# Performance work log

Measured on AMD Instinct MI355X. Metric: run time of the kernel, lower is better.

## Reference

```python
import jax, jax.numpy as jnp
import numpy as np

D_IN, D_OUT, SEQ = 256, 64, 8192

def setup_inputs() -> dict:
    key = jax.random.key(0)
    kx, kq, kk, kv = jax.random.split(key, 4)
    x = jax.random.normal(kx, (SEQ, D_IN), dtype=jnp.float32)
    # original uses torch.rand (uniform [0,1)) for parameters
    W_q = jax.random.uniform(kq, (D_IN, D_OUT), dtype=jnp.float32)
    W_k = jax.random.uniform(kk, (D_IN, D_OUT), dtype=jnp.float32)
    W_v = jax.random.uniform(kv, (D_IN, D_OUT), dtype=jnp.float32)
    return {"x": x, "W_q": W_q, "W_k": W_k, "W_v": W_v}

def reference(x, W_q, W_k, W_v):
    q = x @ W_q          # [S, d_out]
    k = x @ W_k          # [S, d_out]
    v = x @ W_v          # [S, d_out]
    scores = q @ k.T     # [S, S]
    scale = jnp.asarray(D_OUT, scores.dtype) ** 0.5
    weights = jax.nn.softmax(scores / scale, axis=-1)
    return weights @ v   # [S, d_out]
```

## Files before the change

### kernel.cpp

```cpp
#include <hip/hip_runtime.h>
#include <hip/hip_bf16.h>

#define SEQ   8192
#define DIN   256
#define DOUT  64
#define QSCALE 0.1803368801111204f

using bf16x8 = __attribute__((ext_vector_type(8))) short;
using f32x16 = __attribute__((ext_vector_type(16))) float;

__device__ __forceinline__ float exp2f_fast(float x) { return __builtin_amdgcn_exp2f(x); }

__device__ __forceinline__ f32x16 mfma32(bf16x8 a, bf16x8 b, f32x16 c) {
  return __builtin_amdgcn_mfma_f32_32x32x16_bf16(a, b, c, 0, 0, 0);
}

__device__ __forceinline__ unsigned f2bfbits(float f) {
  unsigned u = __builtin_bit_cast(unsigned, f);
  return (u + 0x7fffu + ((u >> 16) & 1u)) >> 16;
}
__device__ __forceinline__ unsigned pkb(float a, float b) {
  return f2bfbits(a) | (f2bfbits(b) << 16);
}
__device__ __forceinline__ float bfhi_f(float v) {
  return __builtin_bit_cast(float, f2bfbits(v) << 16);
}

__global__ __launch_bounds__(256) void qkv_kernel(
    const float* __restrict__ x, const float* __restrict__ wq,
    const float* __restrict__ wk, const float* __restrict__ wv,
    unsigned short* __restrict__ qhi, unsigned short* __restrict__ qlo,
    unsigned short* __restrict__ khi, unsigned short* __restrict__ klo,
    float* __restrict__ vo)
{
  __shared__ float  sxT[DIN * 32];
  __shared__ float4 sw4[DIN * 8];
  const int tid = threadIdx.x;
  const int r0  = blockIdx.x * 32;

  const float4* x4 = (const float4*)x;
  #pragma unroll
  for (int i = 0; i < 8; ++i) {
    int f4  = tid + 256 * i;
    int row = f4 & 31;
    int d4  = f4 >> 5;
    float4 xv = x4[(size_t)(r0 + row) * 64 + d4];
    sxT[(d4 * 4 + 0) * 32 + row] = xv.x;
    sxT[(d4 * 4 + 1) * 32 + row] = xv.y;
    sxT[(d4 * 4 + 2) * 32 + row] = xv.z;
    sxT[(d4 * 4 + 3) * 32 + row] = xv.w;
  }

  const float* wmats[3] = {wq, wk, wv};
  const int r  = tid >> 3;
  const int cg = tid & 7;

  for (int ph = 0; ph < 6; ++ph) {
    int mat = ph >> 1, ch = ph & 1;
    const float4* w4 = (const float4*)wmats[mat];
    #pragma unroll
    for (int i = 0; i < 8; ++i) {
      int f4 = tid + 256 * i;
      int d  = f4 >> 3, c8 = f4 & 7;
      sw4[d * 8 + c8] = w4[d * 16 + ch * 8 + c8];
    }
    __syncthreads();
    float acc[4] = {0.f, 0.f, 0.f, 0.f};
    for (int d = 0; d < DIN; ++d) {
      float  xv = sxT[d * 32 + r];
      float4 w  = sw4[d * 8 + cg];
      acc[0] = fmaf(xv, w.x, acc[0]); acc[1] = fmaf(xv, w.y, acc[1]);
      acc[2] = fmaf(xv, w.z, acc[2]); acc[3] = fmaf(xv, w.w, acc[3]);
    }
    size_t base = (size_t)(r0 + r) * DOUT + ch * 32 + cg * 4;
    if (mat < 2) {
      if (mat == 0) { acc[0]*=QSCALE; acc[1]*=QSCALE; acc[2]*=QSCALE; acc[3]*=QSCALE; }
      ushort4 hv, lv;
      unsigned short* hp = (unsigned short*)&hv;
      unsigned short* lp = (unsigned short*)&lv;
      #pragma unroll
      for (int j = 0; j < 4; ++j) {
        unsigned hb = f2bfbits(acc[j]);
        hp[j] = (unsigned short)hb;
        float fh = __builtin_bit_cast(float, hb << 16);
        lp[j] = (unsigned short)f2bfbits(acc[j] - fh);
      }
      unsigned short* hdst = mat ? khi : qhi;
      unsigned short* ldst = mat ? klo : qlo;
      *(ushort4*)&hdst[base] = hv;
      *(ushort4*)&ldst[base] = lv;
    } else {
      float4 res = {acc[0], acc[1], acc[2], acc[3]};
      *(float4*)&vo[base] = res;
    }
    __syncthreads();
  }
}

__global__ __launch_bounds__(256) void vtrans_kernel(
    const float* __restrict__ v,
    unsigned short* __restrict__ vThi, unsigned short* __restrict__ vTlo)
{
  __shared__ float t[64][65];
  const int tid = threadIdx.x;
  const int r0  = blockIdx.x * 64;
  #pragma unroll
  for (int i = 0; i < 4; ++i) {
    int flat = tid + 256 * i;
    int row = flat >> 4;
    int c4  = flat & 15;
    float4 w = *(const float4*)&v[(size_t)(r0 + row) * 64 + c4 * 4];
    t[row][c4 * 4 + 0] = w.x; t[row][c4 * 4 + 1] = w.y;
    t[row][c4 * 4 + 2] = w.z; t[row][c4 * 4 + 3] = w.w;
  }
  __syncthreads();
  #pragma unroll
  for (int i = 0; i < 2; ++i) {
    int flat = tid + 256 * i;
    int d   = flat >> 3;
    int seg = flat & 7;
    ushort4 h0, h1, l0, l1;
    unsigned short* hp0 = (unsigned short*)&h0; unsigned short* hp1 = (unsigned short*)&h1;
    unsigned short* lp0 = (unsigned short*)&l0; unsigned short* lp1 = (unsigned short*)&l1;
    #pragma unroll
    for (int j = 0; j < 8; ++j) {
      float val = t[seg * 8 + j][d];
      unsigned hb = f2bfbits(val);
      float fh = __builtin_bit_cast(float, hb << 16);
      unsigned lb = f2bfbits(val - fh);
      if (j < 4) { hp0[j] = (unsigned short)hb; lp0[j] = (unsigned short)lb; }
      else       { hp1[j-4] = (unsigned short)hb; lp1[j-4] = (unsigned short)lb; }
    }
    size_t base = (size_t)d * SEQ + r0 + seg * 8;
    *(ushort4*)&vThi[base]     = h0;
    *(ushort4*)&vThi[base + 4] = h1;
    *(ushort4*)&vTlo[base]     = l0;
    *(ushort4*)&vTlo[base + 4] = l1;
  }
}

__global__ __launch_bounds__(512, 2) void attn_mfma_kernel(
    const unsigned short* __restrict__ qhi, const unsigned short* __restrict__ qlo,
    const unsigned short* __restrict__ khi, const unsigned short* __restrict__ klo,
    const unsigned short* __restrict__ vThi, const unsigned short* __restrict__ vTlo,
    float* __restrict__ opart, float2* __restrict__ mlpart, int slice_len)
{
  __shared__ unsigned short sm[2][4][4096];
  const int tid  = threadIdx.x;
  const int lane = tid & 63;
  const int w    = tid >> 6;
  const int qr   = lane & 31;
  const int h    = lane >> 5;
  const int split = blockIdx.y;
  const int j0   = split * slice_len;
  const int qg   = blockIdx.x * 256 + w * 32 + qr;
  const int NT   = slice_len >> 6;

  bf16x8 qh[4], ql[4];
  #pragma unroll
  for (int c = 0; c < 4; ++c) {
    qh[c] = *(const bf16x8*)&qhi[(size_t)qg * 64 + 16 * c + 8 * h];
    ql[c] = *(const bf16x8*)&qlo[(size_t)qg * 64 + 16 * c + 8 * h];
  }

  f32x16 o0, o1;
  #pragma unroll
  for (int i = 0; i < 16; ++i) { o0[i] = 0.f; o1[i] = 0.f; }
  float m = -1.0e30f, l = 0.f;

  const int srow = tid >> 3, sseg = tid & 7;
  const int soff = srow * 64 + ((sseg ^ (srow & 7)) << 3);

  bf16x8 st[4];
  {
    size_t kr  = (size_t)(j0 + srow);
    size_t col = (size_t)(j0 + sseg * 8);
    st[0] = *(const bf16x8*)&khi[kr * 64 + sseg * 8];
    st[1] = *(const bf16x8*)&klo[kr * 64 + sseg * 8];
    st[2] = *(const bf16x8*)&vThi[(size_t)srow * SEQ + col];
    st[3] = *(const bf16x8*)&vTlo[(size_t)srow * SEQ + col];
    #pragma unroll
    for (int a = 0; a < 4; ++a) *(bf16x8*)&sm[0][a][soff] = st[a];
  }
  __syncthreads();

  for (int t = 0; t < NT; ++t) {
    const int b = t & 1;
    bf16x8 nx[4];
    if (t + 1 < NT) {
      size_t kr  = (size_t)(j0 + (t + 1) * 64 + srow);
      size_t col = (size_t)(j0 + (t + 1) * 64 + sseg * 8);
      nx[0] = *(const bf16x8*)&khi[kr * 64 + sseg * 8];
      nx[1] = *(const bf16x8*)&klo[kr * 64 + sseg * 8];
      nx[2] = *(const bf16x8*)&vThi[(size_t)srow * SEQ + col];
      nx[3] = *(const bf16x8*)&vTlo[(size_t)srow * SEQ + col];
    }
    const unsigned short* KH = &sm[b][0][0];
    const unsigned short* KL = &sm[b][1][0];
    const unsigned short* VH = &sm[b][2][0];
    const unsigned short* VL = &sm[b][3][0];

    f32x16 s0, s1;
    #pragma unroll
    for (int i = 0; i < 16; ++i) { s0[i] = 0.f; s1[i] = 0.f; }
    #pragma unroll
    for (int c = 0; c < 4; ++c) {
      int slot = (2 * c + h) ^ (qr & 7);
      int a0 = qr * 64 + slot * 8;
      int a1 = a0 + 32 * 64;
      bf16x8 kh0 = *(const bf16x8*)&KH[a0];
      bf16x8 kh1 = *(const bf16x8*)&KH[a1];
      bf16x8 kl0 = *(const bf16x8*)&KL[a0];
      bf16x8 kl1 = *(const bf16x8*)&KL[a1];
      s0 = mfma32(kh0, qh[c], s0);
      s1 = mfma32(kh1, qh[c], s1);
      s0 = mfma32(kl0, qh[c], s0);
      s1 = mfma32(kl1, qh[c], s1);
      s0 = mfma32(kh0, ql[c], s0);
      s1 = mfma32(kh1, ql[c], s1);
    }

    float pm = s0[0];
    #pragma unroll
    for (int i = 1; i < 16; ++i) pm = fmaxf(pm, s0[i]);
    #pragma unroll
    for (int i = 0; i < 16; ++i) pm = fmaxf(pm, s1[i]);
    pm = fmaxf(pm, __shfl_xor(pm, 32));

    bool need = (pm > m + 40.0f);
    if (__any(need)) {
      float nm = fmaxf(m, pm);
      float r  = exp2f_fast(m - nm);
      #pragma unroll
      for (int i = 0; i < 16; ++i) { o0[i] *= r; o1[i] *= r; }
      l *= r; m = nm;
    }
    #pragma unroll
    for (int i = 0; i < 16; ++i) { s0[i] = exp2f_fast(s0[i] - m); }
    #pragma unroll
    for (int i = 0; i < 16; ++i) { s1[i] = exp2f_fast(s1[i] - m); }
    float ls = 0.f;
    #pragma unroll
    for (int i = 0; i < 16; ++i) ls += s0[i];
    #pragma unroll
    for (int i = 0; i < 16; ++i) ls += s1[i];
    l += ls + __shfl_xor(ls, 32);

    unsigned fw[4][4];
    #pragma unroll
    for (int ti = 0; ti < 2; ++ti) {
      #pragma unroll
      for (int c = 0; c < 2; ++c) {
        const f32x16& S = ti ? s1 : s0;
        unsigned X0 = pkb(S[8*c+0], S[8*c+1]);
        unsigned Y0 = pkb(S[8*c+2], S[8*c+3]);
        unsigned X1 = pkb(S[8*c+4], S[8*c+5]);
        unsigned Y1 = pkb(S[8*c+6], S[8*c+7]);
        unsigned rX0 = __shfl_xor(X0, 32);
        unsigned rY0 = __shfl_xor(Y0, 32);
        unsigned rX1 = __shfl_xor(X1, 32);
        unsigned rY1 = __shfl_xor(Y1, 32);
        fw[ti*2+c][0] = h ? rX1 : X0;
        fw[ti*2+c][1] = h ? rY1 : Y0;
        fw[ti*2+c][2] = h ? X1  : rX0;
        fw[ti*2+c][3] = h ? Y1  : rY0;
      }
    }

    #pragma unroll
    for (int dt = 0; dt < 2; ++dt) {
      f32x16& O = dt ? o1 : o0;
      #pragma unroll
      for (int kc = 0; kc < 4; ++kc) {
        int slot = (2 * kc + h) ^ (qr & 7);
        int addr = (qr + 32 * dt) * 64 + slot * 8;
        uint4 u = {fw[kc][0], fw[kc][1], fw[kc][2], fw[kc][3]};
        bf16x8 pf = __builtin_bit_cast(bf16x8, u);
        bf16x8 vh = *(const bf16x8*)&VH[addr];
        bf16x8 vl = *(const bf16x8*)&VL[addr];
        O = mfma32(vh, pf, O);
        O = mfma32(vl, pf, O);
      }
    }

    __syncthreads();
    if (t + 1 < NT) {
      #pragma unroll
      for (int a = 0; a < 4; ++a) *(bf16x8*)&sm[b ^ 1][a][soff] = nx[a];
    }
    __syncthreads();
  }

  const size_t obase = ((size_t)split * SEQ + qg) * 64;
  #pragma unroll
  for (int b2 = 0; b2 < 4; ++b2) {
    int d0 = 8 * b2 + 4 * h;
    float4 w0 = {o0[4*b2+0], o0[4*b2+1], o0[4*b2+2], o0[4*b2+3]};
    *(float4*)&opart[obase + d0] = w0;
    float4 w1 = {o1[4*b2+0], o1[4*b2+1], o1[4*b2+2], o1[4*b2+3]};
    *(float4*)&opart[obase + 32 + d0] = w1;
  }
  if (h == 0) mlpart[(size_t)split * SEQ + qg] = make_float2(m, l);
}

__global__ __launch_bounds__(256) void combine_kernel(
    const float* __restrict__ opart, const float2* __restrict__ mlpart,
    float* __restrict__ out, int S)
{
  const int tid = threadIdx.x;
  const int row = blockIdx.x * 16 + (tid >> 4);
  const int c4  = tid & 15;
  float mstar = -3.0e38f;
  for (int i = 0; i < S; ++i)
    mstar = fmaxf(mstar, mlpart[(size_t)i * SEQ + row].x);
  float L = 0.f, ax = 0.f, ay = 0.f, az = 0.f, aw = 0.f;
  for (int i = 0; i < S; ++i) {
    float2 ml = mlpart[(size_t)i * SEQ + row];
    float  wgt = exp2f_fast(ml.x - mstar);
    L = fmaf(wgt, ml.y, L);
    float4 ov = ((const float4*)(opart + ((size_t)i * SEQ + row) * DOUT))[c4];
    ax = fmaf(wgt, ov.x, ax); ay = fmaf(wgt, ov.y, ay);
    az = fmaf(wgt, ov.z, az); aw = fmaf(wgt, ov.w, aw);
  }
  float inv = 1.0f / L;
  float4 res = {ax * inv, ay * inv, az * inv, aw * inv};
  ((float4*)(out + (size_t)row * DOUT))[c4] = res;
}

extern "C" void kernel_launch(void* const* d_in, const int* in_sizes, int n_in,
                              void* d_out, int out_size, void* d_ws, size_t ws_size,
                              hipStream_t stream)
{
  const float* x  = (const float*)d_in[0];
  const float* wq = (const float*)d_in[1];
  const float* wk = (const float*)d_in[2];
  const float* wv = (const float*)d_in[3];
  float* out = (float*)d_out;

  char* ws = (char*)d_ws;
  const size_t MB = (size_t)SEQ * DOUT * 2;
  unsigned short* qhi  = (unsigned short*)(ws);
  unsigned short* qlo  = (unsigned short*)(ws + MB);
  unsigned short* khi  = (unsigned short*)(ws + 2 * MB);
  unsigned short* klo  = (unsigned short*)(ws + 3 * MB);
  unsigned short* vThi = (unsigned short*)(ws + 4 * MB);
  unsigned short* vTlo = (unsigned short*)(ws + 5 * MB);
  float* vf32  = (float*)(ws + 6 * MB);
  float* opart = (float*)(ws + 8 * MB);

  int S = 16;
  while (S > 1) {
    size_t need = 8 * MB + ((size_t)S * SEQ * DOUT + (size_t)S * SEQ * 2) * 4;
    if (need <= ws_size) break;
    S >>= 1;
  }
  float2* mlpart = (float2*)(opart + (size_t)S * SEQ * DOUT);
  const int slice_len = SEQ / S;

  qkv_kernel<<<256, 256, 0, stream>>>(x, wq, wk, wv, qhi, qlo, khi, klo, vf32);
  vtrans_kernel<<<SEQ / 64, 256, 0, stream>>>(vf32, vThi, vTlo);
  attn_mfma_kernel<<<dim3(SEQ / 256, S), 512, 0, stream>>>(
      qhi, qlo, khi, klo, vThi, vTlo, opart, mlpart, slice_len);
  combine_kernel<<<SEQ / 16, 256, 0, stream>>>(opart, mlpart, out, S);
}
```

Baseline: 154.2 us.

## Use MFMA for QKV projection, async global-to-LDS staging, two query tiles per wave

The scalar-FMA QKV kernel and separate V transpose kernel are replaced by a weight-split kernel plus an MFMA projection kernel using hi/lo bf16 splits, which writes V transposed directly. The attention kernel now stages K/V tiles with global_load_lds, removing the register round-trip and one barrier per tile. Each wave now handles 64 queries, reusing every LDS K/V fragment across two query tiles, with 256 threads per block. In exchange, register pressure rises, the lo part of Q is reloaded from global memory inside the loop, and the projection scatters narrow 2-byte stores.

```diff
diff --git a/kernel.cpp b/kernel.cpp
--- a/kernel.cpp
+++ b/kernel.cpp
@@ -10,142 +10,141 @@
 using f32x16 = __attribute__((ext_vector_type(16))) float;
 
 __device__ __forceinline__ float exp2f_fast(float x) { return __builtin_amdgcn_exp2f(x); }
-
 __device__ __forceinline__ f32x16 mfma32(bf16x8 a, bf16x8 b, f32x16 c) {
   return __builtin_amdgcn_mfma_f32_32x32x16_bf16(a, b, c, 0, 0, 0);
 }
-
 __device__ __forceinline__ unsigned f2bfbits(float f) {
   unsigned u = __builtin_bit_cast(unsigned, f);
   return (u + 0x7fffu + ((u >> 16) & 1u)) >> 16;
 }
+__device__ __forceinline__ float bfval(unsigned hb) {
+  return __builtin_bit_cast(float, hb << 16);
+}
 __device__ __forceinline__ unsigned pkb(float a, float b) {
   return f2bfbits(a) | (f2bfbits(b) << 16);
 }
-__device__ __forceinline__ float bfhi_f(float v) {
-  return __builtin_bit_cast(float, f2bfbits(v) << 16);
-}
-
-__global__ __launch_bounds__(256) void qkv_kernel(
-    const float* __restrict__ x, const float* __restrict__ wq,
-    const float* __restrict__ wk, const float* __restrict__ wv,
+__device__ __forceinline__ void gl2lds16(const void* g, void* l) {
+  __builtin_amdgcn_global_load_lds(
+      (const __attribute__((address_space(1))) unsigned*)g,
+      (__attribute__((address_space(3))) unsigned*)l, 16, 0, 0);
+}
+__device__ __forceinline__ bf16x8 lds_frag(const unsigned short* base, int row, int slot) {
+  int phys = slot ^ (row & 7);
+  return *(const bf16x8*)&base[row * 64 + phys * 8];
+}
+
+__global__ __launch_bounds__(256) void wconv_kernel(
+    const float* __restrict__ wq, const float* __restrict__ wk, const float* __restrict__ wv,
+    unsigned short* __restrict__ wThi, unsigned short* __restrict__ wTlo)
+{
+  int flat = blockIdx.x * 256 + threadIdx.x;
+  const float* Ws[3] = {wq, wk, wv};
+  #pragma unroll
+  for (int j = 0; j < 6; ++j) {
+    int idx = flat + j * 8192;
+    int m = idx >> 14, rem = idx & 16383;
+    int c = rem >> 8, d = rem & 255;
+    float val = Ws[m][d * 64 + c];
+    unsigned hb = f2bfbits(val);
+    wThi[idx] = (unsigned short)hb;
+    wTlo[idx] = (unsigned short)f2bfbits(val - bfval(hb));
+  }
+}
+
+__global__ __launch_bounds__(128) void qkv_mfma_kernel(
+    const float* __restrict__ x,
+    const unsigned short* __restrict__ wThi, const unsigned short* __restrict__ wTlo,
     unsigned short* __restrict__ qhi, unsigned short* __restrict__ qlo,
     unsigned short* __restrict__ khi, unsigned short* __restrict__ klo,
-    float* __restrict__ vo)
-{
-  __shared__ float  sxT[DIN * 32];
-  __shared__ float4 sw4[DIN * 8];
-  const int tid = threadIdx.x;
-  const int r0  = blockIdx.x * 32;
-
-  const float4* x4 = (const float4*)x;
-  #pragma unroll
-  for (int i = 0; i < 8; ++i) {
-    int f4  = tid + 256 * i;
-    int row = f4 & 31;
-    int d4  = f4 >> 5;
-    float4 xv = x4[(size_t)(r0 + row) * 64 + d4];
-    sxT[(d4 * 4 + 0) * 32 + row] = xv.x;
-    sxT[(d4 * 4 + 1) * 32 + row] = xv.y;
-    sxT[(d4 * 4 + 2) * 32 + row] = xv.z;
-    sxT[(d4 * 4 + 3) * 32 + row] = xv.w;
-  }
-
-  const float* wmats[3] = {wq, wk, wv};
-  const int r  = tid >> 3;
-  const int cg = tid & 7;
-
-  for (int ph = 0; ph < 6; ++ph) {
-    int mat = ph >> 1, ch = ph & 1;
-    const float4* w4 = (const float4*)wmats[mat];
-    #pragma unroll
-    for (int i = 0; i < 8; ++i) {
-      int f4 = tid + 256 * i;
-      int d  = f4 >> 3, c8 = f4 & 7;
-      sw4[d * 8 + c8] = w4[d * 16 + ch * 8 + c8];
-    }
-    __syncthreads();
-    float acc[4] = {0.f, 0.f, 0.f, 0.f};
-    for (int d = 0; d < DIN; ++d) {
-      float  xv = sxT[d * 32 + r];
-      float4 w  = sw4[d * 8 + cg];
-      acc[0] = fmaf(xv, w.x, acc[0]); acc[1] = fmaf(xv, w.y, acc[1]);
-      acc[2] = fmaf(xv, w.z, acc[2]); acc[3] = fmaf(xv, w.w, acc[3]);
-    }
-    size_t base = (size_t)(r0 + r) * DOUT + ch * 32 + cg * 4;
+    unsigned short* __restrict__ vThi, unsigned short* __restrict__ vTlo)
+{
+  const int tid = threadIdx.x, lane = tid & 63, w = tid >> 6;
+  const int qr = lane & 31, h = lane >> 5;
+  const int mat = blockIdx.y;
+  const int r0 = blockIdx.x * 64 + w * 32;
+
+  const unsigned short* wh = &wThi[mat << 14];
+  const unsigned short* wl = &wTlo[mat << 14];
+
+  f32x16 acc0, acc1;
+  #pragma unroll
+  for (int i = 0; i < 16; ++i) { acc0[i] = 0.f; acc1[i] = 0.f; }
+
+  #pragma unroll
+  for (int kc = 0; kc < 16; ++kc) {
+    const float* xp = &x[(size_t)(r0 + qr) * DIN + kc * 16 + 8 * h];
+    float4 xa = *(const float4*)xp;
+    float4 xb = *(const float4*)(xp + 4);
+    union { unsigned short u[8]; bf16x8 v; } ah, al;
+    float xs[8] = {xa.x, xa.y, xa.z, xa.w, xb.x, xb.y, xb.z, xb.w};
+    #pragma unroll
+    for (int j = 0; j < 8; ++j) {
+      unsigned hb = f2bfbits(xs[j]);
+      ah.u[j] = (unsigned short)hb;
+      al.u[j] = (unsigned short)f2bfbits(xs[j] - bfval(hb));
+    }
+    bf16x8 bh0 = *(const bf16x8*)&wh[(size_t)(qr)      * DIN + kc * 16 + 8 * h];
+    bf16x8 bh1 = *(const bf16x8*)&wh[(size_t)(32 + qr) * DIN + kc * 16 + 8 * h];
+    bf16x8 bl0 = *(const bf16x8*)&wl[(size_t)(qr)      * DIN + kc * 16 + 8 * h];
+    bf16x8 bl1 = *(const bf16x8*)&wl[(size_t)(32 + qr) * DIN + kc * 16 + 8 * h];
     if (mat < 2) {
-      if (mat == 0) { acc[0]*=QSCALE; acc[1]*=QSCALE; acc[2]*=QSCALE; acc[3]*=QSCALE; }
-      ushort4 hv, lv;
-      unsigned short* hp = (unsigned short*)&hv;
-      unsigned short* lp = (unsigned short*)&lv;
-      #pragma unroll
-      for (int j = 0; j < 4; ++j) {
-        unsigned hb = f2bfbits(acc[j]);
-        hp[j] = (unsigned short)hb;
-        float fh = __builtin_bit_cast(float, hb << 16);
-        lp[j] = (unsigned short)f2bfbits(acc[j] - fh);
-      }
-      unsigned short* hdst = mat ? khi : qhi;
-      unsigned short* ldst = mat ? klo : qlo;
-      *(ushort4*)&hdst[base] = hv;
-      *(ushort4*)&ldst[base] = lv;
+      acc0 = mfma32(ah.v, bh0, acc0);
+      acc0 = mfma32(al.v, bh0, acc0);
+      acc0 = mfma32(ah.v, bl0, acc0);
+      acc1 = mfma32(ah.v, bh1, acc1);
+      acc1 = mfma32(al.v, bh1, acc1);
+      acc1 = mfma32(ah.v, bl1, acc1);
     } else {
-      float4 res = {acc[0], acc[1], acc[2], acc[3]};
-      *(float4*)&vo[base] = res;
-    }
-    __syncthreads();
-  }
-}
-
-__global__ __launch_bounds__(256) void vtrans_kernel(
-    const float* __restrict__ v,
-    unsigned short* __restrict__ vThi, unsigned short* __restrict__ vTlo)
-{
-  __shared__ float t[64][65];
-  const int tid = threadIdx.x;
-  const int r0  = blockIdx.x * 64;
-  #pragma unroll
-  for (int i = 0; i < 4; ++i) {
-    int flat = tid + 256 * i;
-    int row = flat >> 4;
-    int c4  = flat & 15;
-    float4 w = *(const float4*)&v[(size_t)(r0 + row) * 64 + c4 * 4];
-    t[row][c4 * 4 + 0] = w.x; t[row][c4 * 4 + 1] = w.y;
-    t[row][c4 * 4 + 2] = w.z; t[row][c4 * 4 + 3] = w.w;
-  }
-  __syncthreads();
-  #pragma unroll
-  for (int i = 0; i < 2; ++i) {
-    int flat = tid + 256 * i;
-    int d   = flat >> 3;
-    int seg = flat & 7;
-    ushort4 h0, h1, l0, l1;
-    unsigned short* hp0 = (unsigned short*)&h0; unsigned short* hp1 = (unsigned short*)&h1;
-    unsigned short* lp0 = (unsigned short*)&l0; unsigned short* lp1 = (unsigned short*)&l1;
-    #pragma unroll
-    for (int j = 0; j < 8; ++j) {
-      float val = t[seg * 8 + j][d];
-      unsigned hb = f2bfbits(val);
-      float fh = __builtin_bit_cast(float, hb << 16);
-      unsigned lb = f2bfbits(val - fh);
-      if (j < 4) { hp0[j] = (unsigned short)hb; lp0[j] = (unsigned short)lb; }
-      else       { hp1[j-4] = (unsigned short)hb; lp1[j-4] = (unsigned short)lb; }
-    }
-    size_t base = (size_t)d * SEQ + r0 + seg * 8;
-    *(ushort4*)&vThi[base]     = h0;
-    *(ushort4*)&vThi[base + 4] = h1;
-    *(ushort4*)&vTlo[base]     = l0;
-    *(ushort4*)&vTlo[base + 4] = l1;
-  }
-}
-
-__global__ __launch_bounds__(512, 2) void attn_mfma_kernel(
+      acc0 = mfma32(bh0, ah.v, acc0);
+      acc0 = mfma32(bl0, ah.v, acc0);
+      acc0 = mfma32(bh0, al.v, acc0);
+      acc1 = mfma32(bh1, ah.v, acc1);
+      acc1 = mfma32(bl1, ah.v, acc1);
+      acc1 = mfma32(bh1, al.v, acc1);
+    }
+  }
+
+  if (mat < 2) {
+    unsigned short* oh = mat ? khi : qhi;
+    unsigned short* ol = mat ? klo : qlo;
+    const float scale = (mat == 0) ? QSCALE : 1.0f;
+    #pragma unroll
+    for (int ct = 0; ct < 2; ++ct) {
+      const f32x16& A = ct ? acc1 : acc0;
+      #pragma unroll
+      for (int i = 0; i < 16; ++i) {
+        int r = r0 + (i & 3) + 8 * (i >> 2) + 4 * h;
+        int c = ct * 32 + qr;
+        float val = A[i] * scale;
+        unsigned hb = f2bfbits(val);
+        oh[(size_t)r * DOUT + c] = (unsigned short)hb;
+        ol[(size_t)r * DOUT + c] = (unsigned short)f2bfbits(val - bfval(hb));
+      }
+    }
+  } else {
+    #pragma unroll
+    for (int ct = 0; ct < 2; ++ct) {
+      const f32x16& A = ct ? acc1 : acc0;
+      #pragma unroll
+      for (int i = 0; i < 16; ++i) {
+        int c = ct * 32 + (i & 3) + 8 * (i >> 2) + 4 * h;
+        int r = r0 + qr;
+        float val = A[i];
+        unsigned hb = f2bfbits(val);
+        vThi[(size_t)c * SEQ + r] = (unsigned short)hb;
+        vTlo[(size_t)c * SEQ + r] = (unsigned short)f2bfbits(val - bfval(hb));
+      }
+    }
+  }
+}
+
+__global__ __launch_bounds__(256, 2) void attn_mfma_kernel(
     const unsigned short* __restrict__ qhi, const unsigned short* __restrict__ qlo,
     const unsigned short* __restrict__ khi, const unsigned short* __restrict__ klo,
     const unsigned short* __restrict__ vThi, const unsigned short* __restrict__ vTlo,
     float* __restrict__ opart, float2* __restrict__ mlpart, int slice_len)
 {
-  __shared__ unsigned short sm[2][4][4096];
+  __shared__ __align__(1024) unsigned short smx[2][4][4096];
   const int tid  = threadIdx.x;
   const int lane = tid & 63;
   const int w    = tid >> 6;
@@ -153,154 +152,162 @@
   const int h    = lane >> 5;
   const int split = blockIdx.y;
   const int j0   = split * slice_len;
-  const int qg   = blockIdx.x * 256 + w * 32 + qr;
   const int NT   = slice_len >> 6;
-
-  bf16x8 qh[4], ql[4];
+  const int qg0  = blockIdx.x * 256 + w * 64 + qr;
+  const int qg1  = qg0 + 32;
+
+  bf16x8 qh0[4], qh1[4];
   #pragma unroll
   for (int c = 0; c < 4; ++c) {
-    qh[c] = *(const bf16x8*)&qhi[(size_t)qg * 64 + 16 * c + 8 * h];
-    ql[c] = *(const bf16x8*)&qlo[(size_t)qg * 64 + 16 * c + 8 * h];
-  }
-
-  f32x16 o0, o1;
-  #pragma unroll
-  for (int i = 0; i < 16; ++i) { o0[i] = 0.f; o1[i] = 0.f; }
-  float m = -1.0e30f, l = 0.f;
-
-  const int srow = tid >> 3, sseg = tid & 7;
-  const int soff = srow * 64 + ((sseg ^ (srow & 7)) << 3);
-
-  bf16x8 st[4];
-  {
-    size_t kr  = (size_t)(j0 + srow);
-    size_t col = (size_t)(j0 + sseg * 8);
-    st[0] = *(const bf16x8*)&khi[kr * 64 + sseg * 8];
-    st[1] = *(const bf16x8*)&klo[kr * 64 + sseg * 8];
-    st[2] = *(const bf16x8*)&vThi[(size_t)srow * SEQ + col];
-    st[3] = *(const bf16x8*)&vTlo[(size_t)srow * SEQ + col];
-    #pragma unroll
-    for (int a = 0; a < 4; ++a) *(bf16x8*)&sm[0][a][soff] = st[a];
-  }
+    qh0[c] = *(const bf16x8*)&qhi[(size_t)qg0 * DOUT + c * 16 + 8 * h];
+    qh1[c] = *(const bf16x8*)&qhi[(size_t)qg1 * DOUT + c * 16 + 8 * h];
+  }
+
+  f32x16 o00, o01, o10, o11;
+  #pragma unroll
+  for (int i = 0; i < 16; ++i) { o00[i] = 0.f; o01[i] = 0.f; o10[i] = 0.f; o11[i] = 0.f; }
+  float m0 = -1.0e30f, m1 = -1.0e30f, l0 = 0.f, l1 = 0.f;
+
+  const int srow_l = lane >> 3;
+  const int sslot  = (lane & 7) ^ srow_l;
+
+  auto stage = [&](int t, int nb) {
+    const int r0k = j0 + t * 64;
+    if (w < 2) {
+      const unsigned short* g = (w == 0) ? khi : klo;
+      #pragma unroll
+      for (int i = 0; i < 8; ++i) {
+        int row = 8 * i + srow_l;
+        gl2lds16(&g[(size_t)(r0k + row) * DOUT + sslot * 8], &smx[nb][w][i * 512]);
+      }
+    } else {
+      const unsigned short* g = (w == 2) ? vThi : vTlo;
+      #pragma unroll
+      for (int i = 0; i < 8; ++i) {
+        int row = 8 * i + srow_l;
+        gl2lds16(&g[(size_t)row * SEQ + r0k + sslot * 8], &smx[nb][w][i * 512]);
+      }
+    }
+  };
+
+  stage(0, 0);
   __syncthreads();
 
   for (int t = 0; t < NT; ++t) {
     const int b = t & 1;
-    bf16x8 nx[4];
-    if (t + 1 < NT) {
-      size_t kr  = (size_t)(j0 + (t + 1) * 64 + srow);
-      size_t col = (size_t)(j0 + (t + 1) * 64 + sseg * 8);
-      nx[0] = *(const bf16x8*)&khi[kr * 64 + sseg * 8];
-      nx[1] = *(const bf16x8*)&klo[kr * 64 + sseg * 8];
-      nx[2] = *(const bf16x8*)&vThi[(size_t)srow * SEQ + col];
-      nx[3] = *(const bf16x8*)&vTlo[(size_t)srow * SEQ + col];
-    }
-    const unsigned short* KH = &sm[b][0][0];
-    const unsigned short* KL = &sm[b][1][0];
-    const unsigned short* VH = &sm[b][2][0];
-    const unsigned short* VL = &sm[b][3][0];
-
-    f32x16 s0, s1;
-    #pragma unroll
-    for (int i = 0; i < 16; ++i) { s0[i] = 0.f; s1[i] = 0.f; }
+    if (t + 1 < NT) stage(t + 1, b ^ 1);
+
+    const unsigned short* KH = &smx[b][0][0];
+    const unsigned short* KL = &smx[b][1][0];
+    const unsigned short* VH = &smx[b][2][0];
+    const unsigned short* VL = &smx[b][3][0];
+
+    f32x16 s00, s01, s10, s11;
+    #pragma unroll
+    for (int i = 0; i < 16; ++i) { s00[i] = 0.f; s01[i] = 0.f; s10[i] = 0.f; s11[i] = 0.f; }
     #pragma unroll
     for (int c = 0; c < 4; ++c) {
-      int slot = (2 * c + h) ^ (qr & 7);
-      int a0 = qr * 64 + slot * 8;
-      int a1 = a0 + 32 * 64;
-      bf16x8 kh0 = *(const bf16x8*)&KH[a0];
-      bf16x8 kh1 = *(const bf16x8*)&KH[a1];
-      bf16x8 kl0 = *(const bf16x8*)&KL[a0];
-      bf16x8 kl1 = *(const bf16x8*)&KL[a1];
-      s0 = mfma32(kh0, qh[c], s0);
-      s1 = mfma32(kh1, qh[c], s1);
-      s0 = mfma32(kl0, qh[c], s0);
-      s1 = mfma32(kl1, qh[c], s1);
-      s0 = mfma32(kh0, ql[c], s0);
-      s1 = mfma32(kh1, ql[c], s1);
-    }
-
-    float pm = s0[0];
-    #pragma unroll
-    for (int i = 1; i < 16; ++i) pm = fmaxf(pm, s0[i]);
-    #pragma unroll
-    for (int i = 0; i < 16; ++i) pm = fmaxf(pm, s1[i]);
-    pm = fmaxf(pm, __shfl_xor(pm, 32));
-
-    bool need = (pm > m + 40.0f);
-    if (__any(need)) {
-      float nm = fmaxf(m, pm);
-      float r  = exp2f_fast(m - nm);
-      #pragma unroll
-      for (int i = 0; i < 16; ++i) { o0[i] *= r; o1[i] *= r; }
-      l *= r; m = nm;
-    }
-    #pragma unroll
-    for (int i = 0; i < 16; ++i) { s0[i] = exp2f_fast(s0[i] - m); }
-    #pragma unroll
-    for (int i = 0; i < 16; ++i) { s1[i] = exp2f_fast(s1[i] - m); }
-    float ls = 0.f;
-    #pragma unroll
-    for (int i = 0; i < 16; ++i) ls += s0[i];
-    #pragma unroll
-    for (int i = 0; i < 16; ++i) ls += s1[i];
-    l += ls + __shfl_xor(ls, 32);
-
-    unsigned fw[4][4];
-    #pragma unroll
-    for (int ti = 0; ti < 2; ++ti) {
-      #pragma unroll
-      for (int c = 0; c < 2; ++c) {
-        const f32x16& S = ti ? s1 : s0;
-        unsigned X0 = pkb(S[8*c+0], S[8*c+1]);
-        unsigned Y0 = pkb(S[8*c+2], S[8*c+3]);
-        unsigned X1 = pkb(S[8*c+4], S[8*c+5]);
-        unsigned Y1 = pkb(S[8*c+6], S[8*c+7]);
-        unsigned rX0 = __shfl_xor(X0, 32);
-        unsigned rY0 = __shfl_xor(Y0, 32);
-        unsigned rX1 = __shfl_xor(X1, 32);
-        unsigned rY1 = __shfl_xor(Y1, 32);
-        fw[ti*2+c][0] = h ? rX1 : X0;
-        fw[ti*2+c][1] = h ? rY1 : Y0;
-        fw[ti*2+c][2] = h ? X1  : rX0;
-        fw[ti*2+c][3] = h ? Y1  : rY0;
-      }
-    }
+      bf16x8 kh0 = lds_frag(KH, qr,      2 * c + h);
+      bf16x8 kh1 = lds_frag(KH, qr + 32, 2 * c + h);
+      bf16x8 kl0 = lds_frag(KL, qr,      2 * c + h);
+      bf16x8 kl1 = lds_frag(KL, qr + 32, 2 * c + h);
+      bf16x8 ql0 = *(const bf16x8*)&qlo[(size_t)qg0 * DOUT + c * 16 + 8 * h];
+      bf16x8 ql1 = *(const bf16x8*)&qlo[(size_t)qg1 * DOUT + c * 16 + 8 * h];
+      s00 = mfma32(kh0, qh0[c], s00);  s01 = mfma32(kh1, qh0[c], s01);
+      s10 = mfma32(kh0, qh1[c], s10);  s11 = mfma32(kh1, qh1[c], s11);
+      s00 = mfma32(kl0, qh0[c], s00);  s01 = mfma32(kl1, qh0[c], s01);
+      s10 = mfma32(kl0, qh1[c], s10);  s11 = mfma32(kl1, qh1[c], s11);
+      s00 = mfma32(kh0, ql0, s00);     s01 = mfma32(kh1, ql0, s01);
+      s10 = mfma32(kh0, ql1, s10);     s11 = mfma32(kh1, ql1, s11);
+    }
+
+    unsigned fw0[4][4], fw1[4][4];
+    auto softmax_pack = [&](f32x16& sA, f32x16& sB, f32x16& oA, f32x16& oB,
+                            float& mm, float& ll, unsigned fw[4][4]) {
+      float pm = sA[0];
+      #pragma unroll
+      for (int i = 1; i < 16; ++i) pm = fmaxf(pm, sA[i]);
+      #pragma unroll
+      for (int i = 0; i < 16; ++i) pm = fmaxf(pm, sB[i]);
+      pm = fmaxf(pm, __shfl_xor(pm, 32));
+      if (__any(pm > mm + 40.0f)) {
+        float nm = fmaxf(mm, pm);
+        float r = exp2f_fast(mm - nm);
+        #pragma unroll
+        for (int i = 0; i < 16; ++i) { oA[i] *= r; oB[i] *= r; }
+        ll *= r; mm = nm;
+      }
+      #pragma unroll
+      for (int i = 0; i < 16; ++i) sA[i] = exp2f_fast(sA[i] - mm);
+      #pragma unroll
+      for (int i = 0; i < 16; ++i) sB[i] = exp2f_fast(sB[i] - mm);
+      float ls = 0.f;
+      #pragma unroll
+      for (int i = 0; i < 16; ++i) ls += sA[i] + sB[i];
+      ll += ls + __shfl_xor(ls, 32);
+      #pragma unroll
+      for (int ti = 0; ti < 2; ++ti) {
+        #pragma unroll
+        for (int c = 0; c < 2; ++c) {
+          const f32x16& S = ti ? sB : sA;
+          unsigned X0 = pkb(S[8*c+0], S[8*c+1]);
+          unsigned Y0 = pkb(S[8*c+2], S[8*c+3]);
+          unsigned X1 = pkb(S[8*c+4], S[8*c+5]);
+          unsigned Y1 = pkb(S[8*c+6], S[8*c+7]);
+          unsigned rX0 = __shfl_xor(X0, 32);
+          unsigned rY0 = __shfl_xor(Y0, 32);
+          unsigned rX1 = __shfl_xor(X1, 32);
+          unsigned rY1 = __shfl_xor(Y1, 32);
+          fw[ti*2+c][0] = h ? rX1 : X0;
+          fw[ti*2+c][1] = h ? rY1 : Y0;
+          fw[ti*2+c][2] = h ? X1  : rX0;
+          fw[ti*2+c][3] = h ? Y1  : rY0;
+        }
+      }
+    };
+    softmax_pack(s00, s01, o00, o01, m0, l0, fw0);
+    softmax_pack(s10, s11, o10, o11, m1, l1, fw1);
 
     #pragma unroll
     for (int dt = 0; dt < 2; ++dt) {
-      f32x16& O = dt ? o1 : o0;
+      f32x16& O0 = dt ? o01 : o00;
+      f32x16& O1 = dt ? o11 : o10;
       #pragma unroll
       for (int kc = 0; kc < 4; ++kc) {
-        int slot = (2 * kc + h) ^ (qr & 7);
-        int addr = (qr + 32 * dt) * 64 + slot * 8;
-        uint4 u = {fw[kc][0], fw[kc][1], fw[kc][2], fw[kc][3]};
-        bf16x8 pf = __builtin_bit_cast(bf16x8, u);
-        bf16x8 vh = *(const bf16x8*)&VH[addr];
-        bf16x8 vl = *(const bf16x8*)&VL[addr];
-        O = mfma32(vh, pf, O);
-        O = mfma32(vl, pf, O);
+        bf16x8 vh = lds_frag(VH, qr + 32 * dt, 2 * kc + h);
+        bf16x8 vl = lds_frag(VL, qr + 32 * dt, 2 * kc + h);
+        uint4 u0 = {fw0[kc][0], fw0[kc][1], fw0[kc][2], fw0[kc][3]};
+        uint4 u1 = {fw1[kc][0], fw1[kc][1], fw1[kc][2], fw1[kc][3]};
+        bf16x8 p0 = __builtin_bit_cast(bf16x8, u0);
+        bf16x8 p1 = __builtin_bit_cast(bf16x8, u1);
+        O0 = mfma32(vh, p0, O0);
+        O0 = mfma32(vl, p0, O0);
+        O1 = mfma32(vh, p1, O1);
+        O1 = mfma32(vl, p1, O1);
       }
     }
 
     __syncthreads();
-    if (t + 1 < NT) {
-      #pragma unroll
-      for (int a = 0; a < 4; ++a) *(bf16x8*)&sm[b ^ 1][a][soff] = nx[a];
-    }
-    __syncthreads();
-  }
-
-  const size_t obase = ((size_t)split * SEQ + qg) * 64;
+  }
+
+  const size_t ob0 = ((size_t)split * SEQ + qg0) * DOUT;
+  const size_t ob1 = ((size_t)split * SEQ + qg1) * DOUT;
   #pragma unroll
   for (int b2 = 0; b2 < 4; ++b2) {
     int d0 = 8 * b2 + 4 * h;
-    float4 w0 = {o0[4*b2+0], o0[4*b2+1], o0[4*b2+2], o0[4*b2+3]};
-    *(float4*)&opart[obase + d0] = w0;
-    float4 w1 = {o1[4*b2+0], o1[4*b2+1], o1[4*b2+2], o1[4*b2+3]};
-    *(float4*)&opart[obase + 32 + d0] = w1;
-  }
-  if (h == 0) mlpart[(size_t)split * SEQ + qg] = make_float2(m, l);
+    float4 v00 = {o00[4*b2+0], o00[4*b2+1], o00[4*b2+2], o00[4*b2+3]};
+    float4 v01 = {o01[4*b2+0], o01[4*b2+1], o01[4*b2+2], o01[4*b2+3]};
+    float4 v10 = {o10[4*b2+0], o10[4*b2+1], o10[4*b2+2], o10[4*b2+3]};
+    float4 v11 = {o11[4*b2+0], o11[4*b2+1], o11[4*b2+2], o11[4*b2+3]};
+    *(float4*)&opart[ob0 + d0]      = v00;
+    *(float4*)&opart[ob0 + 32 + d0] = v01;
+    *(float4*)&opart[ob1 + d0]      = v10;
+    *(float4*)&opart[ob1 + 32 + d0] = v11;
+  }
+  if (h == 0) {
+    mlpart[(size_t)split * SEQ + qg0] = make_float2(m0, l0);
+    mlpart[(size_t)split * SEQ + qg1] = make_float2(m1, l1);
+  }
 }
 
 __global__ __launch_bounds__(256) void combine_kernel(
@@ -345,21 +352,23 @@
   unsigned short* klo  = (unsigned short*)(ws + 3 * MB);
   unsigned short* vThi = (unsigned short*)(ws + 4 * MB);
   unsigned short* vTlo = (unsigned short*)(ws + 5 * MB);
-  float* vf32  = (float*)(ws + 6 * MB);
-  float* opart = (float*)(ws + 8 * MB);
+  unsigned short* wThi = (unsigned short*)(ws + 6 * MB);
+  unsigned short* wTlo = (unsigned short*)(ws + 6 * MB + 131072);
+  float* opart = (float*)(ws + 7 * MB);
 
   int S = 16;
   while (S > 1) {
-    size_t need = 8 * MB + ((size_t)S * SEQ * DOUT + (size_t)S * SEQ * 2) * 4;
+    size_t need = 7 * MB + ((size_t)S * SEQ * DOUT + (size_t)S * SEQ * 2) * 4;
     if (need <= ws_size) break;
     S >>= 1;
   }
   float2* mlpart = (float2*)(opart + (size_t)S * SEQ * DOUT);
   const int slice_len = SEQ / S;
 
-  qkv_kernel<<<256, 256, 0, stream>>>(x, wq, wk, wv, qhi, qlo, khi, klo, vf32);
-  vtrans_kernel<<<SEQ / 64, 256, 0, stream>>>(vf32, vThi, vTlo);
-  attn_mfma_kernel<<<dim3(SEQ / 256, S), 512, 0, stream>>>(
+  wconv_kernel<<<32, 256, 0, stream>>>(wq, wk, wv, wThi, wTlo);
+  qkv_mfma_kernel<<<dim3(SEQ / 64, 3), 128, 0, stream>>>(
+      x, wThi, wTlo, qhi, qlo, khi, klo, vThi, vTlo);
+  attn_mfma_kernel<<<dim3(SEQ / 256, S), 256, 0, stream>>>(
       qhi, qlo, khi, klo, vThi, vTlo, opart, mlpart, slice_len);
   combine_kernel<<<SEQ / 16, 256, 0, stream>>>(opart, mlpart, out, S);
 }
```

After: 132.4 us. 14.1% less time.
